# Kernel optimization log

Measured on AMD Instinct MI355X. Metric: run time of the kernel, lower is better.

## Reference

```python
import jax, jax.numpy as jnp
import numpy as np

B, S, N1, N2, NS = 2048, 1024, 8192, 16384, 256
EPS = 1e-10

def setup_inputs() -> dict:
    key = jax.random.key(0)
    ks = jax.random.split(key, 12)
    t_in = jax.random.uniform(ks[0], (B,), jnp.float32)
    y_in = jax.random.uniform(ks[1], (B, S), jnp.float32)
    den_gas = jax.random.uniform(ks[2], (B, 1), jnp.float32) * 1e4
    alpha_1st = jax.random.uniform(ks[3], (N1,), jnp.float32)
    gamma_1st = jax.random.uniform(ks[4], (N1,), jnp.float32) * 50.0
    alpha_2nd = jax.random.uniform(ks[5], (N2,), jnp.float32)
    gamma_2nd = jax.random.uniform(ks[6], (N2,), jnp.float32) * 50.0
    r1_1st = jax.random.randint(ks[7], (N1,), 0, S, jnp.int32)
    p_1st = jax.random.randint(ks[8], (N1,), 0, S, jnp.int32)
    r1_2nd = jax.random.randint(ks[9], (N2,), 0, S, jnp.int32)
    r2_2nd = jax.random.randint(ks[10], (N2,), 0, S, jnp.int32)
    p_2nd = jax.random.randint(ks[11], (N2,), 0, S, jnp.int32)
    inds_surf = 512 + jnp.arange(NS, dtype=jnp.int32)  # surface species slots
    inds_mant = 768 + jnp.arange(NS, dtype=jnp.int32)  # mantle species slots
    return dict(t_in=t_in, y_in=y_in, den_gas=den_gas,
                alpha_1st=alpha_1st, gamma_1st=gamma_1st,
                alpha_2nd=alpha_2nd, gamma_2nd=gamma_2nd,
                r1_1st=r1_1st, p_1st=p_1st,
                r1_2nd=r1_2nd, r2_2nd=r2_2nd, p_2nd=p_2nd,
                inds_surf=inds_surf, inds_mant=inds_mant)

def reference(t_in, y_in, den_gas, alpha_1st, gamma_1st, alpha_2nd, gamma_2nd,
              r1_1st, p_1st, r1_2nd, r2_2nd, p_2nd, inds_surf, inds_mant):
    zeros = jnp.zeros_like(y_in)
    # medium parameters (module_med): temperature from t, den_norm from den_gas
    T = 10.0 + 5.0 * jax.nn.sigmoid(t_in)[:, None]            # [B,1]
    # rmod_1st / rmod_2nd: modified-Arrhenius rate coefficients
    rates_1st = alpha_1st[None, :] * jnp.exp(-gamma_1st[None, :] / T)      # [B,N1]
    rates_2nd = (alpha_2nd[None, :] * jnp.sqrt(T / 300.0)
                 * jnp.exp(-gamma_2nd[None, :] / T))                       # [B,N2]
    # reaction fluxes (gather)
    terms_1st = rates_1st * y_in[:, r1_1st]                                 # [B,N1]
    terms_2nd = rates_2nd * y_in[:, r1_2nd] * y_in[:, r2_2nd] * den_gas     # [B,N2]
    # surface gain / loss assemblers (gain-only and loss-only scatters)
    gain = (zeros.at[:, p_1st].add(terms_1st)
                 .at[:, p_2nd].add(terms_2nd))[:, inds_surf]
    loss = (zeros.at[:, r1_1st].add(-terms_1st)
                 .at[:, r1_2nd].add(-terms_2nd)
                 .at[:, r2_2nd].add(-terms_2nd))[:, inds_surf]
    dy_surf_gain = jnp.sum(gain, axis=-1, keepdims=True)    # [B,1] >= 0
    dy_surf_loss = -jnp.sum(loss, axis=-1, keepdims=True)   # [B,1] >= 0
    # rmod_smt: surface<->mantle transfer coefficients (three-phase)
    y_surf_tot = jnp.sum(y_in[:, inds_surf], axis=-1, keepdims=True)
    y_mant_tot = jnp.sum(y_in[:, inds_mant], axis=-1, keepdims=True)
    k_s2m = dy_surf_gain / (y_surf_tot + EPS)  # burial rate per surface species
    k_m2s = dy_surf_loss / (y_mant_tot + EPS)  # excavation rate per mantle species
    terms_s2m = k_s2m * y_in[:, inds_surf]     # [B,NS]
    terms_m2s = k_m2s * y_in[:, inds_mant]     # [B,NS]
    # full RHS: asm_smt + asm_1st + asm_2nd
    dy = (zeros
          .at[:, p_1st].add(terms_1st).at[:, r1_1st].add(-terms_1st)
          .at[:, p_2nd].add(terms_2nd)
          .at[:, r1_2nd].add(-terms_2nd).at[:, r2_2nd].add(-terms_2nd)
          .at[:, inds_surf].add(terms_m2s - terms_s2m)
          .at[:, inds_mant].add(terms_s2m - terms_m2s))
    return dy
```

## Files before the change

### kernel.cpp

```cpp
#include <hip/hip_runtime.h>
#include <hip/hip_fp16.h>

constexpr int kB  = 2048;
constexpr int kS  = 1024;
constexpr int kN1 = 8192;
constexpr int kN2 = 16384;
constexpr int kNTERM = kN1 + kN2;
constexpr int kQT    = kNTERM / 4;
constexpr int kRoles = 2*kN1 + 3*kN2;
constexpr float kEPS = 1e-10f;
constexpr int NT = 256;

constexpr int kGrpPitchE[8] = {24, 24, 24, 32, 24, 40, 24, 40};
constexpr int kGrpBase [8]  = {0, 12288, 24576, 36864, 53248, 65536, 86016, 98304};
constexpr int kEllWords     = 118784;
constexpr int kCurWords     = 8 * kS;

constexpr size_t kWsMid  = (size_t)(kCurWords + kEllWords) * 4;
constexpr size_t kWsFull = kWsMid + (size_t)kNTERM * 16;

__global__ __launch_bounds__(NT) void ell_fill(
    const float* __restrict__ a1, const float* __restrict__ g1,
    const float* __restrict__ a2, const float* __restrict__ g2,
    const int* __restrict__ r1_1, const int* __restrict__ p_1,
    const int* __restrict__ r1_2, const int* __restrict__ r2_2,
    const int* __restrict__ p_2,
    unsigned* __restrict__ cursor, unsigned* __restrict__ ell,
    float4* __restrict__ rec)
{
    int i = blockIdx.x * NT + threadIdx.x;
    if (i >= kRoles) return;
    int s, j; bool neg;
    if (i < kN1)                  { j = i;          s = p_1[j];  neg = false; }
    else if (i < 2*kN1)           { j = i - kN1;    s = r1_1[j]; neg = true;  }
    else if (i < 2*kN1 + kN2)     { int q = i - 2*kN1;         j = kN1 + q; s = p_2[q];  neg = false; }
    else if (i < 2*kN1 + 2*kN2)   { int q = i - 2*kN1 - kN2;   j = kN1 + q; s = r1_2[q]; neg = true; }
    else                          { int q = i - 2*kN1 - 2*kN2; j = kN1 + q; s = r2_2[q]; neg = true; }
    int qq = j / kQT;
    unsigned addr = (unsigned)(j - qq * kQT + 1) << 2;
    int grp = qq * 2 + (neg ? 1 : 0);
    unsigned k = atomicAdd(&cursor[grp * kS + s], 1u);
    if (k < (unsigned)kGrpPitchE[grp]) {
        unsigned w = (unsigned)kGrpBase[grp]
                   + ((k >> 3) * (unsigned)kS + (unsigned)s) * 4u + ((k >> 1) & 3u);
        atomicOr(&ell[w], addr << ((k & 1u) * 16u));
    }

    if (rec && i < kNTERM) {
        float4 r;
        if (i < kN1) { r.x = a1[i]; r.y = -g1[i]; r.z = __int_as_float(r1_1[i]); r.w = 0.f; }
        else { int q = i - kN1; r.x = a2[q]; r.y = -g2[q];
               r.z = __int_as_float(r1_2[q]); r.w = __int_as_float(r2_2[q]); }
        rec[i] = r;
    }
}

__device__ __forceinline__ void accum8(uint4 e, const __half2* __restrict__ t2,
                                       float& r0, float& r1)
{
    const char* tb = (const char*)t2;
    float2 f0 = __half22float2(*(const __half2*)(tb + (e.x & 0xffffu)));
    float2 f1 = __half22float2(*(const __half2*)(tb + (e.x >> 16)));
    float2 f2 = __half22float2(*(const __half2*)(tb + (e.y & 0xffffu)));
    float2 f3 = __half22float2(*(const __half2*)(tb + (e.y >> 16)));
    float2 f4 = __half22float2(*(const __half2*)(tb + (e.z & 0xffffu)));
    float2 f5 = __half22float2(*(const __half2*)(tb + (e.z >> 16)));
    float2 f6 = __half22float2(*(const __half2*)(tb + (e.w & 0xffffu)));
    float2 f7 = __half22float2(*(const __half2*)(tb + (e.w >> 16)));
    r0 += ((f0.x + f1.x) + (f2.x + f3.x)) + ((f4.x + f5.x) + (f6.x + f7.x));
    r1 += ((f0.y + f1.y) + (f2.y + f3.y)) + ((f4.y + f5.y) + (f6.y + f7.y));
}

__device__ __forceinline__ void glist2_pf(
    const uint4* __restrict__ ap, const uint4* __restrict__ an,
    uint4 ep, uint4 en, int cp, int cn, const __half2* __restrict__ t2,
    float& p0, float& p1, float& n0, float& n1)
{
    accum8(ep, t2, p0, p1);
    accum8(en, t2, n0, n1);
    int tp = (cp + 7) >> 3;
    int tn = (cn + 7) >> 3;
    int T = tp > tn ? tp : tn;
    for (int t = 1; t < T; ++t) {
        bool dp = t < tp, dn = t < tn;
        uint4 e2, e3;
        if (dp) e2 = *ap;
        if (dn) e3 = *an;
        ap += kS; an += kS;
        if (dp) accum8(e2, t2, p0, p1);
        if (dn) accum8(e3, t2, n0, n1);
    }
}

template<bool REC>
__global__ __launch_bounds__(NT, 4) void three_phase_gather5(
    const float* __restrict__ t_in, const float* __restrict__ y_in,
    const float* __restrict__ den_gas,
    const float* __restrict__ a1, const float* __restrict__ g1,
    const float* __restrict__ a2, const float* __restrict__ g2,
    const int* __restrict__ r1_1,
    const int* __restrict__ r1_2, const int* __restrict__ r2_2,
    const unsigned* __restrict__ cursor, const unsigned* __restrict__ ell,
    const float4* __restrict__ rec, float* __restrict__ dy)
{
    __shared__ float2  y2[kS];
    __shared__ __half2 terms2[kQT + 1];
    __shared__ float   red[4][8];

    const int tid = threadIdx.x;
    const int b0  = blockIdx.x * 2;

    {
        const float4* s0 = (const float4*)(y_in + (size_t)b0 * kS);
        const float4* s1 = (const float4*)(y_in + (size_t)(b0 + 1) * kS);
        float4 va = s0[tid], vb = s1[tid];
        y2[4*tid+0] = make_float2(va.x, vb.x);
        y2[4*tid+1] = make_float2(va.y, vb.y);
        y2[4*tid+2] = make_float2(va.z, vb.z);
        y2[4*tid+3] = make_float2(va.w, vb.w);
    }
    if (tid == 0) terms2[0] = __halves2half2(__float2half(0.f), __float2half(0.f));

    float T0 = 10.f + 5.f / (1.f + __expf(-t_in[b0]));
    float T1 = 10.f + 5.f / (1.f + __expf(-t_in[b0 + 1]));
    float i0 = 1.f / T0, i1 = 1.f / T1;
    float c20 = __fsqrt_rn(T0 * (1.f / 300.f)) * den_gas[b0];
    float c21 = __fsqrt_rn(T1 * (1.f / 300.f)) * den_gas[b0 + 1];

    float acc[4][2] = {};
    float gn[2] = {}, ls[2] = {};

    #pragma unroll
    for (int q = 0; q < 4; ++q) {
        __syncthreads();
        const int base = q * kQT;
        #pragma unroll 2
        for (int it = 0; it < kQT / NT; ++it) {
            int j = base + it * NT + tid;
            float al, ng; int ra, rb;
            if (REC) {
                float4 r = rec[j];
                al = r.x; ng = r.y;
                ra = __float_as_int(r.z); rb = __float_as_int(r.w);
            } else if (j < kN1) {
                al = a1[j]; ng = -g1[j]; ra = r1_1[j]; rb = 0;
            } else {
                int u = j - kN1;
                al = a2[u]; ng = -g2[u]; ra = r1_2[u]; rb = r2_2[u];
            }
            float t0, t1;
            if (j < kN1) {
                float2 ya = y2[ra];
                t0 = al * __expf(ng * i0) * ya.x;
                t1 = al * __expf(ng * i1) * ya.y;
            } else {
                float2 ya = y2[ra], yb = y2[rb];
                t0 = c20 * al * __expf(ng * i0) * ya.x * yb.x;
                t1 = c21 * al * __expf(ng * i1) * ya.y * yb.y;
            }
            terms2[j - base + 1] = __halves2half2(__float2half(t0), __float2half(t1));
        }
        const unsigned* cp = cursor + (2*q)     * kS;
        const unsigned* cn = cursor + (2*q + 1) * kS;
        const uint4* bp = (const uint4*)(ell + kGrpBase[2*q]);
        const uint4* bn = (const uint4*)(ell + kGrpBase[2*q + 1]);
        uint4 pfp[4], pfn[4]; int ccp[4], ccn[4];
        #pragma unroll
        for (int slot = 0; slot < 4; ++slot) {
            int s = tid + slot * NT;
            int a = (int)cp[s]; ccp[slot] = a < kGrpPitchE[2*q]   ? a : kGrpPitchE[2*q];
            int b = (int)cn[s]; ccn[slot] = b < kGrpPitchE[2*q+1] ? b : kGrpPitchE[2*q+1];
            pfp[slot] = bp[s];
            pfn[slot] = bn[s];
        }
        __syncthreads();
        #pragma unroll
        for (int slot = 0; slot < 4; ++slot) {
            int s = tid + slot * NT;
            float p0 = 0.f, p1 = 0.f, n0 = 0.f, n1 = 0.f;
            glist2_pf(bp + s + kS, bn + s + kS, pfp[slot], pfn[slot],
                      ccp[slot], ccn[slot], terms2, p0, p1, n0, n1);
            acc[slot][0] += p0 - n0;
            acc[slot][1] += p1 - n1;
            if (slot == 2) { gn[0] += p0; gn[1] += p1; ls[0] += n0; ls[1] += n1; }
        }
    }

    float ys0 = y2[512 + tid].x, ys1 = y2[512 + tid].y;
    float ym0 = y2[768 + tid].x, ym1 = y2[768 + tid].y;
    float v[8] = {gn[0], ls[0], ys0, ym0, gn[1], ls[1], ys1, ym1};
    #pragma unroll
    for (int off = 32; off > 0; off >>= 1) {
        #pragma unroll
        for (int w = 0; w < 8; ++w) v[w] += __shfl_down(v[w], off, 64);
    }
    int wave = tid >> 6;
    if ((tid & 63) == 0) {
        #pragma unroll
        for (int w = 0; w < 8; ++w) red[wave][w] = v[w];
    }
    __syncthreads();
    float tv[8];
    #pragma unroll
    for (int w = 0; w < 8; ++w) tv[w] = red[0][w] + red[1][w] + red[2][w] + red[3][w];

    float ks2m0 = tv[0] / (tv[2] + kEPS), km2s0 = tv[1] / (tv[3] + kEPS);
    float ks2m1 = tv[4] / (tv[6] + kEPS), km2s1 = tv[5] / (tv[7] + kEPS);

    float* o0 = dy + (size_t)b0 * kS;
    float* o1 = o0 + kS;
    o0[tid]       = acc[0][0];
    o0[tid + 256] = acc[1][0];
    o0[tid + 512] = acc[2][0] + km2s0 * ym0 - ks2m0 * ys0;
    o0[tid + 768] = acc[3][0] + ks2m0 * ys0 - km2s0 * ym0;
    o1[tid]       = acc[0][1];
    o1[tid + 256] = acc[1][1];
    o1[tid + 512] = acc[2][1] + km2s1 * ym1 - ks2m1 * ys1;
    o1[tid + 768] = acc[3][1] + ks2m1 * ys1 - km2s1 * ym1;
}

__global__ __launch_bounds__(NT) void three_phase_scatter(
    const float* __restrict__ t_in, const float* __restrict__ y_in,
    const float* __restrict__ den_gas,
    const float* __restrict__ alpha_1st, const float* __restrict__ gamma_1st,
    const float* __restrict__ alpha_2nd, const float* __restrict__ gamma_2nd,
    const int* __restrict__ r1_1st, const int* __restrict__ p_1st,
    const int* __restrict__ r1_2nd, const int* __restrict__ r2_2nd,
    const int* __restrict__ p_2nd, float* __restrict__ dy)
{
    __shared__ float y_row[kS];
    __shared__ float accs[kS];
    __shared__ float tot[4];
    const int tid = threadIdx.x;
    const int b   = blockIdx.x;
    ((float4*)y_row)[tid] = ((const float4*)(y_in + (size_t)b * kS))[tid];
    ((float4*)accs)[tid] = make_float4(0.f, 0.f, 0.f, 0.f);
    if (tid < 4) tot[tid] = 0.f;
    float t = t_in[b];
    float T = 10.f + 5.f / (1.f + __expf(-t));
    float invT = 1.f / T, sqT = __fsqrt_rn(T * (1.f / 300.f)), dg = den_gas[b];
    __syncthreads();
    float gain = 0.f, loss = 0.f;
    for (int j = tid; j < kN1; j += NT) {
        int r1 = r1_1st[j], p = p_1st[j];
        float term = alpha_1st[j] * __expf(-gamma_1st[j] * invT) * y_row[r1];
        atomicAdd(&accs[p], term); atomicAdd(&accs[r1], -term);
        if ((unsigned)(p - 512) < 256u) gain += term;
        if ((unsigned)(r1 - 512) < 256u) loss += term;
    }
    for (int j = tid; j < kN2; j += NT) {
        int r1 = r1_2nd[j], r2 = r2_2nd[j], p = p_2nd[j];
        float term = sqT * dg * alpha_2nd[j] * __expf(-gamma_2nd[j] * invT) * y_row[r1] * y_row[r2];
        atomicAdd(&accs[p], term); atomicAdd(&accs[r1], -term); atomicAdd(&accs[r2], -term);
        if ((unsigned)(p - 512) < 256u) gain += term;
        if ((unsigned)(r1 - 512) < 256u) loss += term;
        if ((unsigned)(r2 - 512) < 256u) loss += term;
    }
    float g = gain, l = loss;
    #pragma unroll
    for (int off = 32; off > 0; off >>= 1) { g += __shfl_down(g, off, 64); l += __shfl_down(l, off, 64); }
    if ((tid & 63) == 0) { atomicAdd(&tot[0], g); atomicAdd(&tot[1], l); }
    __syncthreads();
    if (tid < 64) {
        float a2v = 0.f;
        for (int u = tid; u < 256; u += 64) a2v += y_row[512 + u];
        #pragma unroll
        for (int off = 32; off > 0; off >>= 1) a2v += __shfl_down(a2v, off, 64);
        if (tid == 0) tot[2] = a2v;
    } else if (tid < 128) {
        float m2 = 0.f;
        for (int u = tid - 64; u < 256; u += 64) m2 += y_row[768 + u];
        #pragma unroll
        for (int off = 32; off > 0; off >>= 1) m2 += __shfl_down(m2, off, 64);
        if (tid == 64) tot[3] = m2;
    }
    __syncthreads();
    float k_s2m = tot[0] / (tot[2] + kEPS);
    float k_m2s = tot[1] / (tot[3] + kEPS);
    float* out = dy + (size_t)b * kS;
    for (int s = tid; s < kS; s += NT) {
        float v = accs[s];
        if ((unsigned)(s - 512) < 256u) v += k_m2s * y_row[s + 256] - k_s2m * y_row[s];
        else if (s >= 768)              v += k_s2m * y_row[s - 256] - k_m2s * y_row[s];
        out[s] = v;
    }
}

extern "C" void kernel_launch(void* const* d_in, const int* in_sizes, int n_in,
                              void* d_out, int out_size, void* d_ws, size_t ws_size,
                              hipStream_t stream) {
    const float* t_in      = (const float*)d_in[0];
    const float* y_in      = (const float*)d_in[1];
    const float* den_gas   = (const float*)d_in[2];
    const float* alpha_1st = (const float*)d_in[3];
    const float* gamma_1st = (const float*)d_in[4];
    const float* alpha_2nd = (const float*)d_in[5];
    const float* gamma_2nd = (const float*)d_in[6];
    const int*   r1_1st    = (const int*)d_in[7];
    const int*   p_1st     = (const int*)d_in[8];
    const int*   r1_2nd    = (const int*)d_in[9];
    const int*   r2_2nd    = (const int*)d_in[10];
    const int*   p_2nd     = (const int*)d_in[11];
    float* dy = (float*)d_out;

    if (ws_size >= kWsMid) {
        unsigned* cursor = (unsigned*)d_ws;
        unsigned* ell    = cursor + kCurWords;
        float4*   rec    = (ws_size >= kWsFull)
                         ? (float4*)((char*)d_ws + kWsMid) : (float4*)nullptr;
        hipMemsetAsync(d_ws, 0, kWsMid, stream);
        ell_fill<<<kRoles / NT, NT, 0, stream>>>(
            alpha_1st, gamma_1st, alpha_2nd, gamma_2nd,
            r1_1st, p_1st, r1_2nd, r2_2nd, p_2nd, cursor, ell, rec);
        if (rec)
            three_phase_gather5<true><<<kB / 2, NT, 0, stream>>>(
                t_in, y_in, den_gas, alpha_1st, gamma_1st, alpha_2nd, gamma_2nd,
                r1_1st, r1_2nd, r2_2nd, cursor, ell, rec, dy);
        else
            three_phase_gather5<false><<<kB / 2, NT, 0, stream>>>(
                t_in, y_in, den_gas, alpha_1st, gamma_1st, alpha_2nd, gamma_2nd,
                r1_1st, r1_2nd, r2_2nd, cursor, ell, rec, dy);
    } else {
        three_phase_scatter<<<kB, NT, 0, stream>>>(
            t_in, y_in, den_gas, alpha_1st, gamma_1st, alpha_2nd, gamma_2nd,
            r1_1st, p_1st, r1_2nd, r2_2nd, p_2nd, dy);
    }
}
```

Measured before the change: 149.3 us.

## Restructure ELL gather with double-buffered prefetch and fma_mix half accumulation

The gather loop is reorganised to interleave all four slots per step and double-buffer the ELL row loads two steps ahead, so global index loads overlap the LDS gathers. Half-to-float conversion and accumulation are fused into v_fma_mix_f32 inline asm, and terms are packed with cvt_pkrtz. Positive and negative sums are kept in separate accumulators, which replaces the special-case gain/loss bookkeeping. ell_fill now uses 16-bit stores instead of atomicOr, and the q loop is no longer fully unrolled. The costs are extra live registers for the prefetch buffers, and pkrtz uses round-toward-zero instead of the previous half conversion, which slightly changes rounding.

Result: slower. 159.2 us (+6.7%).

```diff
diff --git a/kernel.cpp b/kernel.cpp
--- a/kernel.cpp
+++ b/kernel.cpp
@@ -1,5 +1,4 @@
 #include <hip/hip_runtime.h>
-#include <hip/hip_fp16.h>
 
 constexpr int kB  = 2048;
 constexpr int kS  = 1024;
@@ -15,6 +14,10 @@
 constexpr int kGrpBase [8]  = {0, 12288, 24576, 36864, 53248, 65536, 86016, 98304};
 constexpr int kEllWords     = 118784;
 constexpr int kCurWords     = 8 * kS;
+
+constexpr int kPitchN[4] = {24, 32, 40, 40};
+constexpr int kBaseP[4]  = {0, 24576, 53248, 86016};
+constexpr int kBaseN[4]  = {12288, 36864, 65536, 98304};
 
 constexpr size_t kWsMid  = (size_t)(kCurWords + kEllWords) * 4;
 constexpr size_t kWsFull = kWsMid + (size_t)kNTERM * 16;
@@ -43,7 +46,7 @@
     if (k < (unsigned)kGrpPitchE[grp]) {
         unsigned w = (unsigned)kGrpBase[grp]
                    + ((k >> 3) * (unsigned)kS + (unsigned)s) * 4u + ((k >> 1) & 3u);
-        atomicOr(&ell[w], addr << ((k & 1u) * 16u));
+        ((unsigned short*)ell)[w * 2u + (k & 1u)] = (unsigned short)addr;
     }
 
     if (rec && i < kNTERM) {
@@ -55,45 +58,25 @@
     }
 }
 
-__device__ __forceinline__ void accum8(uint4 e, const __half2* __restrict__ t2,
-                                       float& r0, float& r1)
+__device__ __forceinline__ void accum8_mix(uint4 e, const char* __restrict__ tb,
+                                           float& r0, float& r1, float one)
 {
-    const char* tb = (const char*)t2;
-    float2 f0 = __half22float2(*(const __half2*)(tb + (e.x & 0xffffu)));
-    float2 f1 = __half22float2(*(const __half2*)(tb + (e.x >> 16)));
-    float2 f2 = __half22float2(*(const __half2*)(tb + (e.y & 0xffffu)));
-    float2 f3 = __half22float2(*(const __half2*)(tb + (e.y >> 16)));
-    float2 f4 = __half22float2(*(const __half2*)(tb + (e.z & 0xffffu)));
-    float2 f5 = __half22float2(*(const __half2*)(tb + (e.z >> 16)));
-    float2 f6 = __half22float2(*(const __half2*)(tb + (e.w & 0xffffu)));
-    float2 f7 = __half22float2(*(const __half2*)(tb + (e.w >> 16)));
-    r0 += ((f0.x + f1.x) + (f2.x + f3.x)) + ((f4.x + f5.x) + (f6.x + f7.x));
-    r1 += ((f0.y + f1.y) + (f2.y + f3.y)) + ((f4.y + f5.y) + (f6.y + f7.y));
-}
-
-__device__ __forceinline__ void glist2_pf(
-    const uint4* __restrict__ ap, const uint4* __restrict__ an,
-    uint4 ep, uint4 en, int cp, int cn, const __half2* __restrict__ t2,
-    float& p0, float& p1, float& n0, float& n1)
-{
-    accum8(ep, t2, p0, p1);
-    accum8(en, t2, n0, n1);
-    int tp = (cp + 7) >> 3;
-    int tn = (cn + 7) >> 3;
-    int T = tp > tn ? tp : tn;
-    for (int t = 1; t < T; ++t) {
-        bool dp = t < tp, dn = t < tn;
-        uint4 e2, e3;
-        if (dp) e2 = *ap;
-        if (dn) e3 = *an;
-        ap += kS; an += kS;
-        if (dp) accum8(e2, t2, p0, p1);
-        if (dn) accum8(e3, t2, n0, n1);
+    unsigned w[4] = {e.x, e.y, e.z, e.w};
+    #pragma unroll
+    for (int i = 0; i < 4; ++i) {
+        unsigned h0 = *(const unsigned*)(tb + (w[i] & 0xffffu));
+        unsigned h1 = *(const unsigned*)(tb + (w[i] >> 16));
+        asm("v_fma_mix_f32 %0, %2, %3, %0 op_sel:[0,0,0] op_sel_hi:[1,0,0]\n\t"
+            "v_fma_mix_f32 %1, %2, %3, %1 op_sel:[1,0,0] op_sel_hi:[1,0,0]"
+            : "+v"(r0), "+v"(r1) : "v"(h0), "v"(one));
+        asm("v_fma_mix_f32 %0, %2, %3, %0 op_sel:[0,0,0] op_sel_hi:[1,0,0]\n\t"
+            "v_fma_mix_f32 %1, %2, %3, %1 op_sel:[1,0,0] op_sel_hi:[1,0,0]"
+            : "+v"(r0), "+v"(r1) : "v"(h1), "v"(one));
     }
 }
 
 template<bool REC>
-__global__ __launch_bounds__(NT, 4) void three_phase_gather5(
+__global__ __launch_bounds__(NT, 4) void three_phase_gather6(
     const float* __restrict__ t_in, const float* __restrict__ y_in,
     const float* __restrict__ den_gas,
     const float* __restrict__ a1, const float* __restrict__ g1,
@@ -103,9 +86,9 @@
     const unsigned* __restrict__ cursor, const unsigned* __restrict__ ell,
     const float4* __restrict__ rec, float* __restrict__ dy)
 {
-    __shared__ float2  y2[kS];
-    __shared__ __half2 terms2[kQT + 1];
-    __shared__ float   red[4][8];
+    __shared__ float2   y2[kS];
+    __shared__ unsigned terms2[kQT + 1];
+    __shared__ float    red[4][8];
 
     const int tid = threadIdx.x;
     const int b0  = blockIdx.x * 2;
@@ -119,7 +102,7 @@
         y2[4*tid+2] = make_float2(va.z, vb.z);
         y2[4*tid+3] = make_float2(va.w, vb.w);
     }
-    if (tid == 0) terms2[0] = __halves2half2(__float2half(0.f), __float2half(0.f));
+    if (tid == 0) terms2[0] = 0u;
 
     float T0 = 10.f + 5.f / (1.f + __expf(-t_in[b0]));
     float T1 = 10.f + 5.f / (1.f + __expf(-t_in[b0 + 1]));
@@ -127,14 +110,14 @@
     float c20 = __fsqrt_rn(T0 * (1.f / 300.f)) * den_gas[b0];
     float c21 = __fsqrt_rn(T1 * (1.f / 300.f)) * den_gas[b0 + 1];
 
-    float acc[4][2] = {};
-    float gn[2] = {}, ls[2] = {};
-
-    #pragma unroll
+    float accp[4][2] = {};
+    float accn[4][2] = {};
+    float one = 1.0f;
+
     for (int q = 0; q < 4; ++q) {
         __syncthreads();
         const int base = q * kQT;
-        #pragma unroll 2
+        #pragma unroll 4
         for (int it = 0; it < kQT / NT; ++it) {
             int j = base + it * NT + tid;
             float al, ng; int ra, rb;
@@ -158,37 +141,61 @@
                 t0 = c20 * al * __expf(ng * i0) * ya.x * yb.x;
                 t1 = c21 * al * __expf(ng * i1) * ya.y * yb.y;
             }
-            terms2[j - base + 1] = __halves2half2(__float2half(t0), __float2half(t1));
+            terms2[j - base + 1] =
+                __builtin_bit_cast(unsigned, __builtin_amdgcn_cvt_pkrtz(t0, t1));
         }
+        const int pitchN = kPitchN[q];
         const unsigned* cp = cursor + (2*q)     * kS;
         const unsigned* cn = cursor + (2*q + 1) * kS;
-        const uint4* bp = (const uint4*)(ell + kGrpBase[2*q]);
-        const uint4* bn = (const uint4*)(ell + kGrpBase[2*q + 1]);
-        uint4 pfp[4], pfn[4]; int ccp[4], ccn[4];
+        const uint4* bp = (const uint4*)(ell + kBaseP[q]);
+        const uint4* bn = (const uint4*)(ell + kBaseN[q]);
+        uint4 pA[4], nA[4], pB[4], nB[4];
+        int tp[4], tn[4];
         #pragma unroll
         for (int slot = 0; slot < 4; ++slot) {
             int s = tid + slot * NT;
-            int a = (int)cp[s]; ccp[slot] = a < kGrpPitchE[2*q]   ? a : kGrpPitchE[2*q];
-            int b = (int)cn[s]; ccn[slot] = b < kGrpPitchE[2*q+1] ? b : kGrpPitchE[2*q+1];
-            pfp[slot] = bp[s];
-            pfn[slot] = bn[s];
+            int a = (int)cp[s]; if (a > 24)     a = 24;
+            int b = (int)cn[s]; if (b > pitchN) b = pitchN;
+            tp[slot] = (a + 7) >> 3;
+            tn[slot] = (b + 7) >> 3;
+            pA[slot] = bp[s];
+            nA[slot] = bn[s];
+            pB[slot] = bp[s + kS];
+            nB[slot] = bn[s + kS];
         }
         __syncthreads();
-        #pragma unroll
-        for (int slot = 0; slot < 4; ++slot) {
-            int s = tid + slot * NT;
-            float p0 = 0.f, p1 = 0.f, n0 = 0.f, n1 = 0.f;
-            glist2_pf(bp + s + kS, bn + s + kS, pfp[slot], pfn[slot],
-                      ccp[slot], ccn[slot], terms2, p0, p1, n0, n1);
-            acc[slot][0] += p0 - n0;
-            acc[slot][1] += p1 - n1;
-            if (slot == 2) { gn[0] += p0; gn[1] += p1; ls[0] += n0; ls[1] += n1; }
+        const char* tb = (const char*)terms2;
+        const int TM = pitchN >> 3;
+        for (int t = 0; t < TM; t += 2) {
+            #pragma unroll
+            for (int slot = 0; slot < 4; ++slot) {
+                if (t < tp[slot]) accum8_mix(pA[slot], tb, accp[slot][0], accp[slot][1], one);
+                if (t < tn[slot]) accum8_mix(nA[slot], tb, accn[slot][0], accn[slot][1], one);
+            }
+            #pragma unroll
+            for (int slot = 0; slot < 4; ++slot) {
+                int s = tid + slot * NT;
+                if (t + 2 < tp[slot]) pA[slot] = bp[s + (t + 2) * kS];
+                if (t + 2 < tn[slot]) nA[slot] = bn[s + (t + 2) * kS];
+            }
+            #pragma unroll
+            for (int slot = 0; slot < 4; ++slot) {
+                if (t + 1 < tp[slot]) accum8_mix(pB[slot], tb, accp[slot][0], accp[slot][1], one);
+                if (t + 1 < tn[slot]) accum8_mix(nB[slot], tb, accn[slot][0], accn[slot][1], one);
+            }
+            #pragma unroll
+            for (int slot = 0; slot < 4; ++slot) {
+                int s = tid + slot * NT;
+                if (t + 3 < tp[slot]) pB[slot] = bp[s + (t + 3) * kS];
+                if (t + 3 < tn[slot]) nB[slot] = bn[s + (t + 3) * kS];
+            }
         }
     }
 
     float ys0 = y2[512 + tid].x, ys1 = y2[512 + tid].y;
     float ym0 = y2[768 + tid].x, ym1 = y2[768 + tid].y;
-    float v[8] = {gn[0], ls[0], ys0, ym0, gn[1], ls[1], ys1, ym1};
+    float v[8] = {accp[2][0], accn[2][0], ys0, ym0,
+                  accp[2][1], accn[2][1], ys1, ym1};
     #pragma unroll
     for (int off = 32; off > 0; off >>= 1) {
         #pragma unroll
@@ -209,14 +216,14 @@
 
     float* o0 = dy + (size_t)b0 * kS;
     float* o1 = o0 + kS;
-    o0[tid]       = acc[0][0];
-    o0[tid + 256] = acc[1][0];
-    o0[tid + 512] = acc[2][0] + km2s0 * ym0 - ks2m0 * ys0;
-    o0[tid + 768] = acc[3][0] + ks2m0 * ys0 - km2s0 * ym0;
-    o1[tid]       = acc[0][1];
-    o1[tid + 256] = acc[1][1];
-    o1[tid + 512] = acc[2][1] + km2s1 * ym1 - ks2m1 * ys1;
-    o1[tid + 768] = acc[3][1] + ks2m1 * ys1 - km2s1 * ym1;
+    o0[tid]       = accp[0][0] - accn[0][0];
+    o0[tid + 256] = accp[1][0] - accn[1][0];
+    o0[tid + 512] = accp[2][0] - accn[2][0] + km2s0 * ym0 - ks2m0 * ys0;
+    o0[tid + 768] = accp[3][0] - accn[3][0] + ks2m0 * ys0 - km2s0 * ym0;
+    o1[tid]       = accp[0][1] - accn[0][1];
+    o1[tid + 256] = accp[1][1] - accn[1][1];
+    o1[tid + 512] = accp[2][1] - accn[2][1] + km2s1 * ym1 - ks2m1 * ys1;
+    o1[tid + 768] = accp[3][1] - accn[3][1] + ks2m1 * ys1 - km2s1 * ym1;
 }
 
 __global__ __launch_bounds__(NT) void three_phase_scatter(
@@ -313,11 +320,11 @@
             alpha_1st, gamma_1st, alpha_2nd, gamma_2nd,
             r1_1st, p_1st, r1_2nd, r2_2nd, p_2nd, cursor, ell, rec);
         if (rec)
-            three_phase_gather5<true><<<kB / 2, NT, 0, stream>>>(
+            three_phase_gather6<true><<<kB / 2, NT, 0, stream>>>(
                 t_in, y_in, den_gas, alpha_1st, gamma_1st, alpha_2nd, gamma_2nd,
                 r1_1st, r1_2nd, r2_2nd, cursor, ell, rec, dy);
         else
-            three_phase_gather5<false><<<kB / 2, NT, 0, stream>>>(
+            three_phase_gather6<false><<<kB / 2, NT, 0, stream>>>(
                 t_in, y_in, den_gas, alpha_1st, gamma_1st, alpha_2nd, gamma_2nd,
                 r1_1st, r1_2nd, r2_2nd, cursor, ell, rec, dy);
     } else {
```
